# Performance work log

Measured on AMD Instinct MI355X. Metric: run time of the kernel, lower is better.

The kernel has to match this reference:

```python
import jax, jax.numpy as jnp
import numpy as np
from jax import lax

N_QUBITS = 4
DEPTH = 1
KERNEL = 4
STRIDE = 2


def _ry(theta):
    # RY(theta) = [[cos(t/2), -sin(t/2)], [sin(t/2), cos(t/2)]] (real matrix)
    c, s = jnp.cos(theta / 2), jnp.sin(theta / 2)
    return jnp.stack([jnp.stack([c, -s]), jnp.stack([s, c])])


def _apply_1q(state, U, w):
    # state: [N, 2,2,2,2]; wire w lives on axis 1+w (wire 0 = most significant, PennyLane convention)
    state = jnp.moveaxis(state, 1 + w, -1)
    state = state @ U.T
    return jnp.moveaxis(state, -1, 1 + w)


def _apply_cnot(state, c, t):
    state = jnp.moveaxis(state, (1 + c, 1 + t), (-2, -1))
    state = jnp.stack([state[..., 0, :], state[..., 1, ::-1]], axis=-2)
    return jnp.moveaxis(state, (-2, -1), (1 + c, 1 + t))


def _circuit(psi, weights):
    # psi: [N, 16] normalized real amplitudes; entire circuit (RY + CNOT) is real
    state = psi.reshape(-1, 2, 2, 2, 2)
    for d in range(DEPTH):
        for i in range(N_QUBITS):
            state = _apply_1q(state, _ry(weights[d, i]), i)
        for i in range(N_QUBITS):
            state = _apply_cnot(state, i, (i + 1) % N_QUBITS)
        for i in range(N_QUBITS):
            state = _apply_1q(state, _ry(weights[d, N_QUBITS + i]), i)
    probs = state * state  # real statevector -> |amp|^2
    z = jnp.array([1.0, -1.0], dtype=state.dtype)
    # <Z_w> for each wire
    return jnp.stack([
        jnp.einsum('nabcd,a->n', probs, z),
        jnp.einsum('nabcd,b->n', probs, z),
        jnp.einsum('nabcd,c->n', probs, z),
        jnp.einsum('nabcd,d->n', probs, z)], axis=-1)  # [N, 4]


def setup_inputs() -> dict:
    key = jax.random.key(0)
    k1, k2 = jax.random.split(key)
    x = jax.random.normal(k1, (8192, 1, 32, 32), dtype=jnp.float32)
    weights = jax.random.normal(k2, (DEPTH, 2 * N_QUBITS), dtype=jnp.float32)
    return {"x": x, "weights": weights}


def reference(x, weights):
    B = x.shape[0]
    # zero-pad right/bottom so truncated border slices become zero-padded amplitude inputs
    xp = jnp.pad(x, ((0, 0), (0, 0), (0, STRIDE), (0, STRIDE)))
    # [B, 16, Hp, Wp]; with C=1 features are the row-major flattened 4x4 patch
    patches = lax.conv_general_dilated_patches(
        xp, (KERNEL, KERNEL), (STRIDE, STRIDE), 'VALID')
    Hp, Wp = patches.shape[2], patches.shape[3]
    P = Hp * Wp
    v = patches.reshape(B, KERNEL * KERNEL, P).transpose(0, 2, 1)
    v = v.reshape(B * P, KERNEL * KERNEL)
    # AmplitudeEmbedding(normalize=True)
    psi = v / jnp.linalg.norm(v, axis=-1, keepdims=True)
    exps = _circuit(psi, weights)           # [B*P, 4]
    return exps.reshape(B, P * N_QUBITS)    # patch-major concat, matches torch.cat order
```

## Files before the change

### kernel.cpp

```cpp
#include <hip/hip_runtime.h>
#include <math.h>


#define TS 34

#define RY(M, C, S)                                                    \
    {                                                                  \
        _Pragma("unroll") for (int k = 0; k < 16; ++k) {               \
            if ((k & (M)) == 0) {                                      \
                float a0 = st[k], a1 = st[k | (M)];                    \
                st[k]       = (C) * a0 - (S) * a1;                     \
                st[k | (M)] = (S) * a0 + (C) * a1;                     \
            }                                                          \
        }                                                              \
    }

#define CNOT(MC, MT)                                                   \
    {                                                                  \
        _Pragma("unroll") for (int k = 0; k < 16; ++k) {               \
            if ((k & (MC)) != 0 && (k & (MT)) == 0) {                  \
                float t = st[k];                                       \
                st[k] = st[k | (MT)];                                  \
                st[k | (MT)] = t;                                      \
            }                                                          \
        }                                                              \
    }

#define MEAS(M, CF, SF, OUTV)                                          \
    {                                                                  \
        float A = 0.f, X = 0.f;                                        \
        _Pragma("unroll") for (int k = 0; k < 16; ++k) {               \
            if ((k & (M)) == 0) {                                      \
                A += q[k | (M)];                                       \
                X = fmaf(st[k], st[k | (M)], X);                       \
            }                                                          \
        }                                                              \
        float Zb = T - 2.0f * A;                                       \
        OUTV = ((CF) * Zb - (SF) * (2.0f * X)) * inv;                  \
    }

__global__ __launch_bounds__(256) void quanv_kernel(
    const float* __restrict__ x, const float* __restrict__ w,
    float* __restrict__ out)
{
    __shared__ float tile[34 * TS];
    __shared__ float trig[16];

    const int tid = threadIdx.x;
    const int b = blockIdx.x;

    if (tid < 4) {
        float t = w[tid] * 0.5f;
        trig[tid]     = cosf(t);
        trig[4 + tid] = sinf(t);
    } else if (tid < 8) {
        float t = w[tid];
        trig[4 + tid] = cosf(t);
        trig[8 + tid] = sinf(t);
    }

    const float4 xin = *(const float4*)(x + (size_t)b * 1024 + (tid << 2));
    {
        int row = tid >> 3, col = (tid & 7) << 2;
        float* dst = &tile[row * TS + col];
        *(float2*)(dst)     = make_float2(xin.x, xin.y);
        *(float2*)(dst + 2) = make_float2(xin.z, xin.w);
    }
    if (tid < 68) {
        tile[32 * TS + tid] = 0.f;
    } else if (tid < 132) {
        int k = tid - 68;
        tile[(k >> 1) * TS + 32 + (k & 1)] = 0.f;
    }
    __syncthreads();

    const int py = tid >> 4, px = tid & 15;
    const float* pp = &tile[(py << 1) * TS + (px << 1)];
    float st[16];
#pragma unroll
    for (int dr = 0; dr < 4; ++dr) {
        float2 u0 = *(const float2*)(pp + dr * TS);
        float2 u1 = *(const float2*)(pp + dr * TS + 2);
        st[dr * 4 + 0] = u0.x;
        st[dr * 4 + 1] = u0.y;
        st[dr * 4 + 2] = u1.x;
        st[dr * 4 + 3] = u1.y;
    }

    const float c0 = trig[0], c1 = trig[1], c2 = trig[2], c3 = trig[3];
    const float s0 = trig[4], s1 = trig[5], s2 = trig[6], s3 = trig[7];
    const float cf0 = trig[8],  cf1 = trig[9],  cf2 = trig[10], cf3 = trig[11];
    const float sf0 = trig[12], sf1 = trig[13], sf2 = trig[14], sf3 = trig[15];

    RY(8, c0, s0)
    RY(4, c1, s1)
    RY(2, c2, s2)
    RY(1, c3, s3)

    CNOT(8, 4)
    CNOT(4, 2)
    CNOT(2, 1)
    CNOT(1, 8)

    float q[16];
#pragma unroll
    for (int k = 0; k < 16; ++k) q[k] = st[k] * st[k];
    float T = ((q[0] + q[1]) + (q[2] + q[3])) + ((q[4] + q[5]) + (q[6] + q[7])) +
              (((q[8] + q[9]) + (q[10] + q[11])) + ((q[12] + q[13]) + (q[14] + q[15])));
    float inv = 1.0f / T;

    float e0, e1, e2, e3;
    MEAS(8, cf0, sf0, e0)
    MEAS(4, cf1, sf1, e1)
    MEAS(2, cf2, sf2, e2)
    MEAS(1, cf3, sf3, e3)

    *(float4*)(out + (size_t)b * 1024 + (tid << 2)) = make_float4(e0, e1, e2, e3);
}

extern "C" void kernel_launch(void* const* d_in, const int* in_sizes, int n_in,
                              void* d_out, int out_size, void* d_ws, size_t ws_size,
                              hipStream_t stream) {
    const float* x = (const float*)d_in[0];
    const float* w = (const float*)d_in[1];
    float* out = (float*)d_out;
    const int B = in_sizes[0] >> 10;
    quanv_kernel<<<B, 256, 0, stream>>>(x, w, out);
}
```

Baseline: 89.99 us.

## Drop shared-memory tile, load patches directly, precompute trig in separate kernel

Removes the LDS tile staging and __syncthreads; each thread now reads its 4x4 patch straight from global memory (cached), with bounds checks standing in for the zero padding. Trig values are computed once by a tiny pre-kernel into the workspace instead of per block. The Z-expectation reduction is rebuilt as a butterfly of sums and differences that shares partial sums. This trades the coalesced float4 load and LDS reuse for overlapping uncoalesced float2 global loads, and adds a second kernel launch.

Measured after the change: 90.49 us. No clear change (+0.6%).

```diff
diff --git a/kernel.cpp b/kernel.cpp
--- a/kernel.cpp
+++ b/kernel.cpp
@@ -1,8 +1,6 @@
 #include <hip/hip_runtime.h>
 #include <math.h>
 
-
-#define TS 34
 
 #define RY(M, C, S)                                                    \
     {                                                                  \
@@ -26,96 +24,102 @@
         }                                                              \
     }
 
-#define MEAS(M, CF, SF, OUTV)                                          \
-    {                                                                  \
-        float A = 0.f, X = 0.f;                                        \
-        _Pragma("unroll") for (int k = 0; k < 16; ++k) {               \
-            if ((k & (M)) == 0) {                                      \
-                A += q[k | (M)];                                       \
-                X = fmaf(st[k], st[k | (M)], X);                       \
-            }                                                          \
-        }                                                              \
-        float Zb = T - 2.0f * A;                                       \
-        OUTV = ((CF) * Zb - (SF) * (2.0f * X)) * inv;                  \
+__global__ void trig_kernel(const float* __restrict__ w, float* __restrict__ t) {
+    int i = threadIdx.x;
+    if (i < 4) {
+        float h = w[i] * 0.5f;
+        t[i]      = cosf(h);
+        t[4 + i]  = sinf(h);
+        float f = w[4 + i];
+        t[8 + i]  = cosf(f);
+        t[12 + i] = 2.0f * sinf(f);
     }
+}
 
 __global__ __launch_bounds__(256) void quanv_kernel(
-    const float* __restrict__ x, const float* __restrict__ w,
+    const float* __restrict__ x, const float* __restrict__ trig,
     float* __restrict__ out)
 {
-    __shared__ float tile[34 * TS];
-    __shared__ float trig[16];
-
     const int tid = threadIdx.x;
     const int b = blockIdx.x;
+    const int py = tid >> 4, px = tid & 15;
 
-    if (tid < 4) {
-        float t = w[tid] * 0.5f;
-        trig[tid]     = cosf(t);
-        trig[4 + tid] = sinf(t);
-    } else if (tid < 8) {
-        float t = w[tid];
-        trig[4 + tid] = cosf(t);
-        trig[8 + tid] = sinf(t);
-    }
+    const float* img = x + ((size_t)b << 10);
+    const int c0 = px << 1;
 
-    const float4 xin = *(const float4*)(x + (size_t)b * 1024 + (tid << 2));
-    {
-        int row = tid >> 3, col = (tid & 7) << 2;
-        float* dst = &tile[row * TS + col];
-        *(float2*)(dst)     = make_float2(xin.x, xin.y);
-        *(float2*)(dst + 2) = make_float2(xin.z, xin.w);
-    }
-    if (tid < 68) {
-        tile[32 * TS + tid] = 0.f;
-    } else if (tid < 132) {
-        int k = tid - 68;
-        tile[(k >> 1) * TS + 32 + (k & 1)] = 0.f;
-    }
-    __syncthreads();
-
-    const int py = tid >> 4, px = tid & 15;
-    const float* pp = &tile[(py << 1) * TS + (px << 1)];
     float st[16];
 #pragma unroll
     for (int dr = 0; dr < 4; ++dr) {
-        float2 u0 = *(const float2*)(pp + dr * TS);
-        float2 u1 = *(const float2*)(pp + dr * TS + 2);
+        const int r = (py << 1) + dr;
+        float2 u0 = make_float2(0.f, 0.f);
+        float2 u1 = make_float2(0.f, 0.f);
+        if (r < 32) {
+            const float* rp = img + (r << 5) + c0;
+            u0 = *(const float2*)rp;
+            if (c0 < 30) u1 = *(const float2*)(rp + 2);
+        }
         st[dr * 4 + 0] = u0.x;
         st[dr * 4 + 1] = u0.y;
         st[dr * 4 + 2] = u1.x;
         st[dr * 4 + 3] = u1.y;
     }
 
-    const float c0 = trig[0], c1 = trig[1], c2 = trig[2], c3 = trig[3];
-    const float s0 = trig[4], s1 = trig[5], s2 = trig[6], s3 = trig[7];
-    const float cf0 = trig[8],  cf1 = trig[9],  cf2 = trig[10], cf3 = trig[11];
-    const float sf0 = trig[12], sf1 = trig[13], sf2 = trig[14], sf3 = trig[15];
+    const float4 ch  = ((const float4*)trig)[0];
+    const float4 sh  = ((const float4*)trig)[1];
+    const float4 cf  = ((const float4*)trig)[2];
+    const float4 sf2 = ((const float4*)trig)[3];
 
-    RY(8, c0, s0)
-    RY(4, c1, s1)
-    RY(2, c2, s2)
-    RY(1, c3, s3)
+    RY(8, ch.x, sh.x)
+    RY(4, ch.y, sh.y)
+    RY(2, ch.z, sh.z)
+    RY(1, ch.w, sh.w)
 
     CNOT(8, 4)
     CNOT(4, 2)
     CNOT(2, 1)
     CNOT(1, 8)
 
-    float q[16];
+    float p[16];
 #pragma unroll
-    for (int k = 0; k < 16; ++k) q[k] = st[k] * st[k];
-    float T = ((q[0] + q[1]) + (q[2] + q[3])) + ((q[4] + q[5]) + (q[6] + q[7])) +
-              (((q[8] + q[9]) + (q[10] + q[11])) + ((q[12] + q[13]) + (q[14] + q[15])));
+    for (int k = 0; k < 16; ++k) p[k] = st[k] * st[k];
+
+    float sA[8], dA[8];
+#pragma unroll
+    for (int i = 0; i < 8; ++i) {
+        sA[i] = p[2 * i] + p[2 * i + 1];
+        dA[i] = p[2 * i] - p[2 * i + 1];
+    }
+    float Z1 = ((dA[0] + dA[1]) + (dA[2] + dA[3])) +
+               ((dA[4] + dA[5]) + (dA[6] + dA[7]));
+    float sB[4], dB[4];
+#pragma unroll
+    for (int j = 0; j < 4; ++j) {
+        sB[j] = sA[2 * j] + sA[2 * j + 1];
+        dB[j] = sA[2 * j] - sA[2 * j + 1];
+    }
+    float Z2 = (dB[0] + dB[1]) + (dB[2] + dB[3]);
+    float sC0 = sB[0] + sB[1], dC0 = sB[0] - sB[1];
+    float sC1 = sB[2] + sB[3], dC1 = sB[2] - sB[3];
+    float Z4 = dC0 + dC1;
+    float T  = sC0 + sC1;
+    float Z8 = sC0 - sC1;
     float inv = 1.0f / T;
 
-    float e0, e1, e2, e3;
-    MEAS(8, cf0, sf0, e0)
-    MEAS(4, cf1, sf1, e1)
-    MEAS(2, cf2, sf2, e2)
-    MEAS(1, cf3, sf3, e3)
+    float X8 = 0.f, X4 = 0.f, X2 = 0.f, X1 = 0.f;
+#pragma unroll
+    for (int k = 0; k < 16; ++k) {
+        if ((k & 8) == 0) X8 = fmaf(st[k], st[k | 8], X8);
+        if ((k & 4) == 0) X4 = fmaf(st[k], st[k | 4], X4);
+        if ((k & 2) == 0) X2 = fmaf(st[k], st[k | 2], X2);
+        if ((k & 1) == 0) X1 = fmaf(st[k], st[k | 1], X1);
+    }
 
-    *(float4*)(out + (size_t)b * 1024 + (tid << 2)) = make_float4(e0, e1, e2, e3);
+    const float e0 = (cf.x * Z8 - sf2.x * X8) * inv;
+    const float e1 = (cf.y * Z4 - sf2.y * X4) * inv;
+    const float e2 = (cf.z * Z2 - sf2.z * X2) * inv;
+    const float e3 = (cf.w * Z1 - sf2.w * X1) * inv;
+
+    *(float4*)(out + ((size_t)b << 10) + (tid << 2)) = make_float4(e0, e1, e2, e3);
 }
 
 extern "C" void kernel_launch(void* const* d_in, const int* in_sizes, int n_in,
@@ -124,6 +128,9 @@
     const float* x = (const float*)d_in[0];
     const float* w = (const float*)d_in[1];
     float* out = (float*)d_out;
+    float* trig = (float*)d_ws;
     const int B = in_sizes[0] >> 10;
-    quanv_kernel<<<B, 256, 0, stream>>>(x, w, out);
+
+    trig_kernel<<<1, 64, 0, stream>>>(w, trig);
+    quanv_kernel<<<B, 256, 0, stream>>>(x, trig, out);
 }
```
